# Kernel tuning notes

Measured on AMD Instinct MI355X. Metric: run time of the kernel, lower is better.

Reference implementation:

```python
import jax, jax.numpy as jnp
import numpy as np

N = 50000        # num nodes
E = 800000       # num edges (before self loops)
IN = 128         # in_channels
HID = 64         # hidden_channels
HEADS = 3        # num_heads
OUT = 32         # out_channels
SLOPE = 0.2      # PyG GATConv default negative_slope
HC = HEADS * HID


def setup_inputs() -> dict:
    key = jax.random.key(0)
    ks = jax.random.split(key, 12)

    def glorot(k, shape, fan_in):
        return jax.random.normal(k, shape, dtype=jnp.float32) / np.float32(np.sqrt(fan_in))

    x = jax.random.normal(ks[0], (N, IN), dtype=jnp.float32)
    edge_index = jax.random.randint(ks[1], (2, E), 0, N, dtype=jnp.int32)
    return {
        "x": x,
        "edge_index": edge_index,
        "W1": glorot(ks[2], (IN, HC), IN),
        "a_src1": glorot(ks[3], (HEADS, HID), HID),
        "a_dst1": glorot(ks[4], (HEADS, HID), HID),
        "b1": jnp.zeros((HC,), jnp.float32),
        "W2": glorot(ks[5], (HC, HC), HC),
        "a_src2": glorot(ks[6], (HEADS, HID), HID),
        "a_dst2": glorot(ks[7], (HEADS, HID), HID),
        "b2": jnp.zeros((HC,), jnp.float32),
        "Wf1": glorot(ks[8], (HC, 64), HC),
        "bf1": jnp.zeros((64,), jnp.float32),
        "Wf2": glorot(ks[9], (64, OUT), 64),
        "bf2": jnp.zeros((OUT,), jnp.float32),
        "num_nodes": N,
    }


def gat_conv(x, src, dst, W, a_src, a_dst, b, num_nodes):
    """PyG-style GATConv: linear -> edge score (LeakyReLU) -> segment softmax
    over incoming edges per destination -> weighted scatter-sum -> concat heads."""
    H, C = a_src.shape
    h = (x @ W).reshape(num_nodes, H, C)              # [N,H,C]
    alpha_s = jnp.einsum("nhc,hc->nh", h, a_src)      # [N,H]
    alpha_d = jnp.einsum("nhc,hc->nh", h, a_dst)      # [N,H]
    e = jax.nn.leaky_relu(alpha_s[src] + alpha_d[dst], SLOPE)  # [E',H]
    # numerically stable segment softmax over destination nodes
    m = jax.lax.stop_gradient(jax.ops.segment_max(e, dst, num_segments=num_nodes))
    ex = jnp.exp(e - m[dst])
    denom = jax.ops.segment_sum(ex, dst, num_segments=num_nodes)
    alpha = ex / (denom[dst] + 1e-16)                 # [E',H]
    msg = h[src] * alpha[:, :, None]                  # [E',H,C]
    out = jax.ops.segment_sum(msg, dst, num_segments=num_nodes)  # [N,H,C]
    return out.reshape(num_nodes, H * C) + b


def reference(x, edge_index, W1, a_src1, a_dst1, b1, W2, a_src2, a_dst2, b2,
              Wf1, bf1, Wf2, bf2, num_nodes):
    # add self loops (PyG GATConv default)
    loops = jnp.arange(num_nodes, dtype=edge_index.dtype)
    src = jnp.concatenate([edge_index[0], loops])
    dst = jnp.concatenate([edge_index[1], loops])

    h = gat_conv(x, src, dst, W1, a_src1, a_dst1, b1, num_nodes)
    h = jax.nn.elu(h)
    # dropout is identity in eval mode
    h = gat_conv(h, src, dst, W2, a_src2, a_dst2, b2, num_nodes)
    h = jax.nn.elu(h)
    h = h @ Wf1 + bf1
    return h @ Wf2 + bf2
```

## Files before the change

kernel.cpp:

```cpp
#include <hip/hip_runtime.h>

#define N_NODES 50000
#define E_EDGES 800000
#define EP (E_EDGES + N_NODES)
#define IN_CH 128
#define HID 64
#define HEADS 3
#define HC 192
#define OUT_CH 32
#define SLOPE 0.2f

#define N4 12500
#define SCAN_BLK 49

#define MB_XCONV 6250
#define MB_W1 (MB_XCONV + 96)
#define MB_W2 (MB_W1 + 144)
#define MB_FOLD (MB_W2 + 25)
#define MB_HIST (MB_FOLD + 3321)

typedef __attribute__((ext_vector_type(8))) short bf16x8;
typedef __attribute__((ext_vector_type(4))) float f32x4;

__device__ __forceinline__ unsigned short f2bf(float f) {
    unsigned int u = __float_as_uint(f);
    u = (u + 0x7fffu + ((u >> 16) & 1u)) >> 16;
    return (unsigned short)u;
}
__device__ __forceinline__ float loF(unsigned int u) { return __uint_as_float(u << 16); }
__device__ __forceinline__ float hiF(unsigned int u) { return __uint_as_float(u & 0xFFFF0000u); }


__global__ __launch_bounds__(256) void mega_pre_kernel(
    const float* __restrict__ x, unsigned short* __restrict__ xb,
    const float* __restrict__ W1, unsigned short* __restrict__ W1T,
    const float* __restrict__ W2, unsigned short* __restrict__ W2T,
    const float* __restrict__ Wf1, const float* __restrict__ bf1,
    const float* __restrict__ Wf2, const float* __restrict__ bf2,
    float* __restrict__ Wf, float* __restrict__ bf,
    const int* __restrict__ ei, int* __restrict__ cnt) {
    int b = blockIdx.x, t = threadIdx.x;
    if (b < MB_XCONV) {
        int i = b * 256 + t;
        float4 v = ((const float4*)x)[i];
        uint2 o;
        o.x = (unsigned int)f2bf(v.x) | ((unsigned int)f2bf(v.y) << 16);
        o.y = (unsigned int)f2bf(v.z) | ((unsigned int)f2bf(v.w) << 16);
        ((uint2*)xb)[i] = o;
    } else if (b < MB_W1) {
        int bb = b - MB_XCONV;
        int k = (bb & 3) * 32 + (t & 31);
        int n = (bb >> 2) * 8 + (t >> 5);
        W1T[n * IN_CH + k] = f2bf(W1[(size_t)k * HC + n]);
    } else if (b < MB_W2) {
        int bb = b - MB_W1;
        int k = (bb % 6) * 32 + (t & 31);
        int n = (bb / 6) * 8 + (t >> 5);
        W2T[n * HC + k] = f2bf(W2[(size_t)k * HC + n]);
    } else if (b < MB_FOLD) {
        int id = (b - MB_W2) * 256 + t;
        if (id < HC * OUT_CH) {
            int i = id / OUT_CH, j = id % OUT_CH;
            float s = 0.f;
            for (int k = 0; k < 64; ++k) s += Wf1[i * 64 + k] * Wf2[k * OUT_CH + j];
            Wf[id] = s;
        } else if (id < HC * OUT_CH + OUT_CH) {
            int j = id - HC * OUT_CH;
            float s = bf2[j];
            for (int k = 0; k < 64; ++k) s += bf1[k] * Wf2[k * OUT_CH + j];
            bf[j] = s;
        }
    } else {
        int i = (b - MB_FOLD) * 256 + t;
        if (i < EP) {
            int d = (i < E_EDGES) ? ei[E_EDGES + i] : (i - E_EDGES);
            atomicAdd(&cnt[d], 1);
        }
    }
}


__global__ __launch_bounds__(256) void scan_local_kernel(int* __restrict__ cnt,
                                                         int* __restrict__ offs,
                                                         int* __restrict__ bsum) {
    __shared__ int s[256];
    int t = threadIdx.x;
    int g = blockIdx.x * 256 + t;
    int4 v = make_int4(0, 0, 0, 0);
    if (g < N4) v = ((const int4*)cnt)[g];
    int sum = v.x + v.y + v.z + v.w;
    s[t] = sum; __syncthreads();
    #pragma unroll
    for (int o = 1; o < 256; o <<= 1) {
        int u = (t >= o) ? s[t - o] : 0;
        __syncthreads();
        s[t] += u;
        __syncthreads();
    }
    int ex = s[t] - sum;
    if (g < N4) {
        int4 w;
        w.x = ex;
        w.y = ex + v.x;
        w.z = ex + v.x + v.y;
        w.w = ex + v.x + v.y + v.z;
        ((int4*)offs)[g] = w;
        ((int4*)cnt)[g] = make_int4(0, 0, 0, 0);
    }
    if (t == 255) bsum[blockIdx.x] = s[255];
}

__global__ __launch_bounds__(256) void scan_add_kernel(int* __restrict__ offs,
                                                       const int* __restrict__ bsum) {
    int lane = threadIdx.x & 63;
    int orig = (lane < SCAN_BLK) ? bsum[lane] : 0;
    int v = orig;
    #pragma unroll
    for (int o = 1; o < 64; o <<= 1) {
        int u = __shfl_up(v, o);
        if (lane >= o) v += u;
    }
    int add = __shfl(v, blockIdx.x) - __shfl(orig, blockIdx.x);
    int total = __shfl(v, SCAN_BLK - 1);
    int g = blockIdx.x * 256 + threadIdx.x;
    if (g < N4) {
        int4 w = ((int4*)offs)[g];
        w.x += add; w.y += add; w.z += add; w.w += add;
        ((int4*)offs)[g] = w;
    }
    if (blockIdx.x == 0 && threadIdx.x == 0) offs[N_NODES] = total;
}

__global__ void scatter_kernel(const int* __restrict__ ei, const int* __restrict__ offs,
                               int* __restrict__ cnt, int* __restrict__ src_sort) {
    int i = blockIdx.x * 256 + threadIdx.x;
    if (i >= EP) return;
    int s_, d_;
    if (i < E_EDGES) { s_ = ei[i]; d_ = ei[E_EDGES + i]; }
    else             { s_ = d_ = i - E_EDGES; }
    int slot = atomicAdd(&cnt[d_], 1);
    src_sort[offs[d_] + slot] = s_;
}


#define GBM 128
#define GBK 64
#define LDA 72
#define CS_STR 200

template <int K>
__global__ __launch_bounds__(256) void gemm_mfma_kernel(
    const unsigned short* __restrict__ Ab, const unsigned short* __restrict__ Wt,
    const float* __restrict__ a_src, const float* __restrict__ a_dst,
    unsigned short* __restrict__ Hb, float* __restrict__ AS, float* __restrict__ AD) {
    __shared__ __align__(16) unsigned char smem[51200];
    unsigned short (*As)[LDA] = (unsigned short (*)[LDA])smem;
    unsigned short (*Bs)[LDA] = (unsigned short (*)[LDA])(smem + GBM * LDA * 2);
    int tid = threadIdx.x;
    int wid = tid >> 6, lane = tid & 63;
    int l15 = lane & 15, l4 = lane >> 4;
    int m0 = blockIdx.x * GBM;
    int sr = tid >> 3, sc = (tid & 7) * 8;

    f32x4 acc[2][12];
    #pragma unroll
    for (int m = 0; m < 2; ++m)
        #pragma unroll
        for (int n = 0; n < 12; ++n) acc[m][n] = (f32x4){0.f, 0.f, 0.f, 0.f};

    for (int kb = 0; kb < K; kb += GBK) {
        #pragma unroll
        for (int i = 0; i < 4; ++i) {
            int r = sr + 32 * i, grow = m0 + r;
            uint4 v = make_uint4(0, 0, 0, 0);
            if (grow < N_NODES) v = *(const uint4*)&Ab[(size_t)grow * K + kb + sc];
            *(uint4*)&As[r][sc] = v;
        }
        #pragma unroll
        for (int i = 0; i < 6; ++i) {
            int n = sr + 32 * i;
            uint4 v = *(const uint4*)&Wt[(size_t)n * K + kb + sc];
            *(uint4*)&Bs[n][sc] = v;
        }
        __syncthreads();
        #pragma unroll
        for (int ks = 0; ks < 2; ++ks) {
            int ko = ks * 32 + l4 * 8;
            bf16x8 a0 = *(const bf16x8*)&As[wid * 32 + l15][ko];
            bf16x8 a1 = *(const bf16x8*)&As[wid * 32 + 16 + l15][ko];
            #pragma unroll
            for (int n = 0; n < 12; ++n) {
                bf16x8 b = *(const bf16x8*)&Bs[n * 16 + l15][ko];
                acc[0][n] = __builtin_amdgcn_mfma_f32_16x16x32_bf16(a0, b, acc[0][n], 0, 0, 0);
                acc[1][n] = __builtin_amdgcn_mfma_f32_16x16x32_bf16(a1, b, acc[1][n], 0, 0, 0);
            }
        }
        __syncthreads();
    }

    float asv[12], adv[12];
    #pragma unroll
    for (int n = 0; n < 12; ++n) {
        asv[n] = a_src[n * 16 + l15];
        adv[n] = a_dst[n * 16 + l15];
    }
    #pragma unroll
    for (int m = 0; m < 2; ++m)
        #pragma unroll
        for (int r = 0; r < 4; ++r) {
            float ps[3], pd[3];
            #pragma unroll
            for (int h = 0; h < 3; ++h) {
                float s = 0.f, d = 0.f;
                #pragma unroll
                for (int j = 0; j < 4; ++j) {
                    float v = acc[m][4 * h + j][r];
                    s += v * asv[4 * h + j];
                    d += v * adv[4 * h + j];
                }
                #pragma unroll
                for (int o = 1; o < 16; o <<= 1) { s += __shfl_xor(s, o); d += __shfl_xor(d, o); }
                ps[h] = s; pd[h] = d;
            }
            if (l15 == 0) {
                int grow = m0 + wid * 32 + m * 16 + l4 * 4 + r;
                if (grow < N_NODES) {
                    #pragma unroll
                    for (int h = 0; h < 3; ++h) {
                        AS[grow * 3 + h] = ps[h];
                        AD[grow * 3 + h] = pd[h];
                    }
                }
            }
        }

    unsigned short* Cw = (unsigned short*)smem + wid * 32 * CS_STR;
    #pragma unroll
    for (int m = 0; m < 2; ++m)
        #pragma unroll
        for (int n = 0; n < 12; ++n)
            #pragma unroll
            for (int r = 0; r < 4; ++r)
                Cw[(m * 16 + l4 * 4 + r) * CS_STR + n * 16 + l15] = f2bf(acc[m][n][r]);
    __syncthreads();
    #pragma unroll
    for (int i = 0; i < 12; ++i) {
        int c = lane + 64 * i;
        int row = c / 24, off = c % 24;
        int grow = m0 + wid * 32 + row;
        if (grow < N_NODES) {
            uint4 v = *(const uint4*)&Cw[row * CS_STR + off * 8];
            *(uint4*)&Hb[(size_t)grow * HC + off * 8] = v;
        }
    }
}


__global__ __launch_bounds__(256) void aggregate_kernel(
    const int* __restrict__ src_sort, const int* __restrict__ offs,
    const float* __restrict__ AS, const float* __restrict__ AD,
    const unsigned short* __restrict__ Hb, const float* __restrict__ bias,
    unsigned short* __restrict__ Aout) {
    int w = blockIdx.x * 4 + (threadIdx.x >> 6);
    if (w >= N_NODES) return;
    int lane = threadIdx.x & 63;
    int g = lane >> 4, l = lane & 15, h3 = lane & 3;
    int beg = offs[w], end = offs[w + 1];

    float mx = -1e30f;
    for (int p0 = beg; p0 < end; p0 += 16) {
        int p = p0 + (lane >> 2);
        bool vld = (p < end) && (h3 < 3);
        int s_ = vld ? src_sort[p] : 0;
        float a = vld ? AS[s_ * 3 + h3] : -1e30f;
        mx = fmaxf(mx, a);
    }
    mx = fmaxf(mx, __shfl_xor(mx, 4));
    mx = fmaxf(mx, __shfl_xor(mx, 8));
    mx = fmaxf(mx, __shfl_xor(mx, 16));
    mx = fmaxf(mx, __shfl_xor(mx, 32));
    float ad = (l < 3) ? AD[w * 3 + l] : 0.f;
    float sm = mx + ad;
    float m = fmaxf(sm, SLOPE * sm);

    int c0 = l * 12;
    int h0 = c0 >> 6, h1 = (c0 + 4) >> 6, h2 = (c0 + 8) >> 6;
    float A0 = 0.f, A1 = 0.f, A2 = 0.f, A3 = 0.f;
    float B0 = 0.f, B1 = 0.f, B2 = 0.f, B3 = 0.f;
    float C0 = 0.f, C1 = 0.f, C2 = 0.f, C3 = 0.f;
    float den = 0.f;

    for (int p0 = beg; p0 < end; p0 += 4) {
        int p = p0 + g;
        bool pv = p < end;
        int pc = pv ? p : end - 1;
        int s_ = src_sort[pc];
        float e = 0.f;
        if (l < 3) {
            float v = AS[s_ * 3 + l] + ad;
            v = fmaxf(v, SLOPE * v);
            e = pv ? __expf(v - m) : 0.f;
        }
        den += e;
        float w0 = __shfl(e, g * 16 + h0);
        float w1 = __shfl(e, g * 16 + h1);
        float w2 = __shfl(e, g * 16 + h2);
        const unsigned short* hr = Hb + (unsigned)s_ * HC + c0;
        uint2 v0 = *(const uint2*)hr;
        uint2 v1 = *(const uint2*)(hr + 4);
        uint2 v2 = *(const uint2*)(hr + 8);
        A0 += w0 * loF(v0.x); A1 += w0 * hiF(v0.x); A2 += w0 * loF(v0.y); A3 += w0 * hiF(v0.y);
        B0 += w1 * loF(v1.x); B1 += w1 * hiF(v1.x); B2 += w1 * loF(v1.y); B3 += w1 * hiF(v1.y);
        C0 += w2 * loF(v2.x); C1 += w2 * hiF(v2.x); C2 += w2 * loF(v2.y); C3 += w2 * hiF(v2.y);
    }

    #pragma unroll
    for (int o = 16; o < 64; o <<= 1) {
        A0 += __shfl_xor(A0, o); A1 += __shfl_xor(A1, o); A2 += __shfl_xor(A2, o); A3 += __shfl_xor(A3, o);
        B0 += __shfl_xor(B0, o); B1 += __shfl_xor(B1, o); B2 += __shfl_xor(B2, o); B3 += __shfl_xor(B3, o);
        C0 += __shfl_xor(C0, o); C1 += __shfl_xor(C1, o); C2 += __shfl_xor(C2, o); C3 += __shfl_xor(C3, o);
        den += __shfl_xor(den, o);
    }
    float i0 = 1.f / (__shfl(den, h0) + 1e-16f);
    float i1 = 1.f / (__shfl(den, h1) + 1e-16f);
    float i2 = 1.f / (__shfl(den, h2) + 1e-16f);

    if (lane < 16) {
        float4 bi0 = *(const float4*)&bias[c0];
        float4 bi1 = *(const float4*)&bias[c0 + 4];
        float4 bi2 = *(const float4*)&bias[c0 + 8];
        A0 = A0 * i0 + bi0.x; A1 = A1 * i0 + bi0.y; A2 = A2 * i0 + bi0.z; A3 = A3 * i0 + bi0.w;
        B0 = B0 * i1 + bi1.x; B1 = B1 * i1 + bi1.y; B2 = B2 * i1 + bi1.z; B3 = B3 * i1 + bi1.w;
        C0 = C0 * i2 + bi2.x; C1 = C1 * i2 + bi2.y; C2 = C2 * i2 + bi2.z; C3 = C3 * i2 + bi2.w;
        A0 = (A0 > 0.f) ? A0 : (__expf(A0) - 1.f);
        A1 = (A1 > 0.f) ? A1 : (__expf(A1) - 1.f);
        A2 = (A2 > 0.f) ? A2 : (__expf(A2) - 1.f);
        A3 = (A3 > 0.f) ? A3 : (__expf(A3) - 1.f);
        B0 = (B0 > 0.f) ? B0 : (__expf(B0) - 1.f);
        B1 = (B1 > 0.f) ? B1 : (__expf(B1) - 1.f);
        B2 = (B2 > 0.f) ? B2 : (__expf(B2) - 1.f);
        B3 = (B3 > 0.f) ? B3 : (__expf(B3) - 1.f);
        C0 = (C0 > 0.f) ? C0 : (__expf(C0) - 1.f);
        C1 = (C1 > 0.f) ? C1 : (__expf(C1) - 1.f);
        C2 = (C2 > 0.f) ? C2 : (__expf(C2) - 1.f);
        C3 = (C3 > 0.f) ? C3 : (__expf(C3) - 1.f);
        unsigned short* op = Aout + (size_t)w * HC + c0;
        uint2 o0, o1, o2;
        o0.x = (unsigned int)f2bf(A0) | ((unsigned int)f2bf(A1) << 16);
        o0.y = (unsigned int)f2bf(A2) | ((unsigned int)f2bf(A3) << 16);
        o1.x = (unsigned int)f2bf(B0) | ((unsigned int)f2bf(B1) << 16);
        o1.y = (unsigned int)f2bf(B2) | ((unsigned int)f2bf(B3) << 16);
        o2.x = (unsigned int)f2bf(C0) | ((unsigned int)f2bf(C1) << 16);
        o2.y = (unsigned int)f2bf(C2) | ((unsigned int)f2bf(C3) << 16);
        *(uint2*)op = o0;
        *(uint2*)(op + 4) = o1;
        *(uint2*)(op + 8) = o2;
    }
}


__global__ __launch_bounds__(256) void mlp_kernel(const unsigned short* __restrict__ act,
                                                  const float* __restrict__ Wf,
                                                  const float* __restrict__ bf,
                                                  float* __restrict__ out) {
    __shared__ float sW[HC * OUT_CH];
    __shared__ float sA[32 * 193];
    __shared__ float sb[OUT_CH];
    int tid = threadIdx.x;
    for (int i = tid; i < HC * OUT_CH; i += 256) sW[i] = Wf[i];
    if (tid < OUT_CH) sb[tid] = bf[tid];
    int n0 = blockIdx.x * 32;
    for (int i = tid; i < 32 * HC / 4; i += 256) {
        int r = i / 48, c4 = i % 48;
        int n = n0 + r;
        uint2 v = make_uint2(0, 0);
        if (n < N_NODES) v = *(const uint2*)&act[(size_t)n * HC + c4 * 4];
        float* dst = &sA[r * 193 + c4 * 4];
        dst[0] = loF(v.x); dst[1] = hiF(v.x); dst[2] = loF(v.y); dst[3] = hiF(v.y);
    }
    __syncthreads();
    int r = tid >> 3, jg = tid & 7;
    float a0 = sb[jg * 4 + 0], a1 = sb[jg * 4 + 1], a2 = sb[jg * 4 + 2], a3 = sb[jg * 4 + 3];
    #pragma unroll 4
    for (int k = 0; k < HC; ++k) {
        float xv = sA[r * 193 + k];
        float4 wv = *(const float4*)&sW[k * OUT_CH + jg * 4];
        a0 += xv * wv.x; a1 += xv * wv.y; a2 += xv * wv.z; a3 += xv * wv.w;
    }
    int n = n0 + r;
    if (n < N_NODES) {
        float4 v = make_float4(a0, a1, a2, a3);
        *(float4*)&out[(size_t)n * OUT_CH + jg * 4] = v;
    }
}


extern "C" void kernel_launch(void* const* d_in, const int* in_sizes, int n_in,
                              void* d_out, int out_size, void* d_ws, size_t ws_size,
                              hipStream_t stream) {
    (void)in_sizes; (void)n_in; (void)out_size; (void)ws_size;
    const float* x   = (const float*)d_in[0];
    const int*   ei  = (const int*)d_in[1];
    const float* W1  = (const float*)d_in[2];
    const float* as1 = (const float*)d_in[3];
    const float* ad1 = (const float*)d_in[4];
    const float* b1  = (const float*)d_in[5];
    const float* W2  = (const float*)d_in[6];
    const float* as2 = (const float*)d_in[7];
    const float* ad2 = (const float*)d_in[8];
    const float* b2  = (const float*)d_in[9];
    const float* Wf1 = (const float*)d_in[10];
    const float* bf1 = (const float*)d_in[11];
    const float* Wf2 = (const float*)d_in[12];
    const float* bf2 = (const float*)d_in[13];
    float* out = (float*)d_out;

    char* ws = (char*)d_ws;
    size_t off = 0;
    auto alloc = [&](size_t b) { size_t o = off; off += (b + 255) & ~(size_t)255; return o; };
    unsigned short* XB  = (unsigned short*)(ws + alloc((size_t)N_NODES * IN_CH * 2));
    unsigned short* W1T = (unsigned short*)(ws + alloc((size_t)HC * IN_CH * 2));
    unsigned short* W2T = (unsigned short*)(ws + alloc((size_t)HC * HC * 2));
    unsigned short* HB  = (unsigned short*)(ws + alloc((size_t)N_NODES * HC * 2));
    unsigned short* ACT = (unsigned short*)(ws + alloc((size_t)N_NODES * HC * 2));
    int*   SRC  = (int*)  (ws + alloc((size_t)(EP + 64) * 4));
    float* AS   = (float*)(ws + alloc((size_t)N_NODES * 3 * 4));
    float* AD   = (float*)(ws + alloc((size_t)N_NODES * 3 * 4));
    int*   OFFS = (int*)  (ws + alloc((size_t)(N_NODES + 4) * 4));
    int*   CNT  = (int*)  (ws + alloc((size_t)N_NODES * 4));
    int*   BSUM = (int*)  (ws + alloc((size_t)256 * 4));
    float* WF   = (float*)(ws + alloc((size_t)HC * OUT_CH * 4));
    float* BF   = (float*)(ws + alloc((size_t)OUT_CH * 4));

    int eb = (EP + 255) / 256;
    int gmb = (N_NODES + GBM - 1) / GBM;

    hipMemsetAsync(CNT, 0, (size_t)N_NODES * 4, stream);
    mega_pre_kernel<<<MB_HIST, 256, 0, stream>>>(x, XB, W1, W1T, W2, W2T,
                                                 Wf1, bf1, Wf2, bf2, WF, BF, ei, CNT);
    scan_local_kernel<<<SCAN_BLK, 256, 0, stream>>>(CNT, OFFS, BSUM);
    scan_add_kernel<<<SCAN_BLK, 256, 0, stream>>>(OFFS, BSUM);
    scatter_kernel<<<eb, 256, 0, stream>>>(ei, OFFS, CNT, SRC);

    gemm_mfma_kernel<IN_CH><<<gmb, 256, 0, stream>>>(XB, W1T, as1, ad1, HB, AS, AD);
    aggregate_kernel<<<(N_NODES + 3) / 4, 256, 0, stream>>>(SRC, OFFS, AS, AD, HB, b1, ACT);
    gemm_mfma_kernel<HC><<<gmb, 256, 0, stream>>>(ACT, W2T, as2, ad2, HB, AS, AD);
    aggregate_kernel<<<(N_NODES + 3) / 4, 256, 0, stream>>>(SRC, OFFS, AS, AD, HB, b2, ACT);
    mlp_kernel<<<(N_NODES + 31) / 32, 256, 0, stream>>>(ACT, WF, BF, out);
}
```

Before: 307.4 us.

## Split GAT aggregation across heads with one wave per node-head pair

The aggregation kernel now launches one wavefront per (node, head) instead of one per node. Each lane group accumulates a 4-channel slice of a single head, and the next source index is prefetched one iteration ahead. This removes the shuffles that broadcast weights across heads and wastes fewer lanes on exp work, while giving three times as many waves for latency hiding. The cost is that src_sort and the offsets are re-read three times, and each gather touches only an 8-byte slice of the bf16 row, so cache line use per wave is poorer.

```diff
diff --git a/kernel.cpp b/kernel.cpp
--- a/kernel.cpp
+++ b/kernel.cpp
@@ -12,6 +12,7 @@
 
 #define N4 12500
 #define SCAN_BLK 49
+#define NGRP 12500
 
 #define MB_XCONV 6250
 #define MB_W1 (MB_XCONV + 96)
@@ -261,100 +262,64 @@
     const float* __restrict__ AS, const float* __restrict__ AD,
     const unsigned short* __restrict__ Hb, const float* __restrict__ bias,
     unsigned short* __restrict__ Aout) {
-    int w = blockIdx.x * 4 + (threadIdx.x >> 6);
-    if (w >= N_NODES) return;
+    int h = blockIdx.x / NGRP;
+    int g4 = blockIdx.x - h * NGRP;
+    int w = g4 * 4 + (threadIdx.x >> 6);
     int lane = threadIdx.x & 63;
-    int g = lane >> 4, l = lane & 15, h3 = lane & 3;
+    int slot = lane >> 4, l = lane & 15;
     int beg = offs[w], end = offs[w + 1];
+    float ad = AD[w * 3 + h];
 
     float mx = -1e30f;
-    for (int p0 = beg; p0 < end; p0 += 16) {
-        int p = p0 + (lane >> 2);
-        bool vld = (p < end) && (h3 < 3);
-        int s_ = vld ? src_sort[p] : 0;
-        float a = vld ? AS[s_ * 3 + h3] : -1e30f;
-        mx = fmaxf(mx, a);
-    }
-    mx = fmaxf(mx, __shfl_xor(mx, 4));
-    mx = fmaxf(mx, __shfl_xor(mx, 8));
-    mx = fmaxf(mx, __shfl_xor(mx, 16));
-    mx = fmaxf(mx, __shfl_xor(mx, 32));
-    float ad = (l < 3) ? AD[w * 3 + l] : 0.f;
+    for (int p = beg + lane; p < end; p += 64) {
+        int s_ = src_sort[p];
+        mx = fmaxf(mx, AS[s_ * 3 + h]);
+    }
+    #pragma unroll
+    for (int o = 1; o < 64; o <<= 1) mx = fmaxf(mx, __shfl_xor(mx, o));
     float sm = mx + ad;
     float m = fmaxf(sm, SLOPE * sm);
 
-    int c0 = l * 12;
-    int h0 = c0 >> 6, h1 = (c0 + 4) >> 6, h2 = (c0 + 8) >> 6;
-    float A0 = 0.f, A1 = 0.f, A2 = 0.f, A3 = 0.f;
-    float B0 = 0.f, B1 = 0.f, B2 = 0.f, B3 = 0.f;
-    float C0 = 0.f, C1 = 0.f, C2 = 0.f, C3 = 0.f;
-    float den = 0.f;
-
+    int coff = h * 64 + l * 4;
+    float a0 = 0.f, a1 = 0.f, a2 = 0.f, a3 = 0.f, den = 0.f;
+    int p = beg + slot;
+    int s_ = src_sort[(p < end) ? p : (end - 1)];
     for (int p0 = beg; p0 < end; p0 += 4) {
-        int p = p0 + g;
-        bool pv = p < end;
-        int pc = pv ? p : end - 1;
-        int s_ = src_sort[pc];
-        float e = 0.f;
-        if (l < 3) {
-            float v = AS[s_ * 3 + l] + ad;
-            v = fmaxf(v, SLOPE * v);
-            e = pv ? __expf(v - m) : 0.f;
-        }
+        int pn = p0 + 4 + slot;
+        int sn = src_sort[(pn < end) ? pn : (end - 1)];
+        bool pv = (p0 + slot) < end;
+        float v = AS[s_ * 3 + h] + ad;
+        v = fmaxf(v, SLOPE * v);
+        float e = pv ? __expf(v - m) : 0.f;
         den += e;
-        float w0 = __shfl(e, g * 16 + h0);
-        float w1 = __shfl(e, g * 16 + h1);
-        float w2 = __shfl(e, g * 16 + h2);
-        const unsigned short* hr = Hb + (unsigned)s_ * HC + c0;
-        uint2 v0 = *(const uint2*)hr;
-        uint2 v1 = *(const uint2*)(hr + 4);
-        uint2 v2 = *(const uint2*)(hr + 8);
-        A0 += w0 * loF(v0.x); A1 += w0 * hiF(v0.x); A2 += w0 * loF(v0.y); A3 += w0 * hiF(v0.y);
-        B0 += w1 * loF(v1.x); B1 += w1 * hiF(v1.x); B2 += w1 * loF(v1.y); B3 += w1 * hiF(v1.y);
-        C0 += w2 * loF(v2.x); C1 += w2 * hiF(v2.x); C2 += w2 * loF(v2.y); C3 += w2 * hiF(v2.y);
+        uint2 hv = *(const uint2*)&Hb[(unsigned)s_ * HC + coff];
+        a0 += e * loF(hv.x); a1 += e * hiF(hv.x);
+        a2 += e * loF(hv.y); a3 += e * hiF(hv.y);
+        s_ = sn;
     }
 
     #pragma unroll
     for (int o = 16; o < 64; o <<= 1) {
-        A0 += __shfl_xor(A0, o); A1 += __shfl_xor(A1, o); A2 += __shfl_xor(A2, o); A3 += __shfl_xor(A3, o);
-        B0 += __shfl_xor(B0, o); B1 += __shfl_xor(B1, o); B2 += __shfl_xor(B2, o); B3 += __shfl_xor(B3, o);
-        C0 += __shfl_xor(C0, o); C1 += __shfl_xor(C1, o); C2 += __shfl_xor(C2, o); C3 += __shfl_xor(C3, o);
+        a0 += __shfl_xor(a0, o); a1 += __shfl_xor(a1, o);
+        a2 += __shfl_xor(a2, o); a3 += __shfl_xor(a3, o);
         den += __shfl_xor(den, o);
     }
-    float i0 = 1.f / (__shfl(den, h0) + 1e-16f);
-    float i1 = 1.f / (__shfl(den, h1) + 1e-16f);
-    float i2 = 1.f / (__shfl(den, h2) + 1e-16f);
 
     if (lane < 16) {
-        float4 bi0 = *(const float4*)&bias[c0];
-        float4 bi1 = *(const float4*)&bias[c0 + 4];
-        float4 bi2 = *(const float4*)&bias[c0 + 8];
-        A0 = A0 * i0 + bi0.x; A1 = A1 * i0 + bi0.y; A2 = A2 * i0 + bi0.z; A3 = A3 * i0 + bi0.w;
-        B0 = B0 * i1 + bi1.x; B1 = B1 * i1 + bi1.y; B2 = B2 * i1 + bi1.z; B3 = B3 * i1 + bi1.w;
-        C0 = C0 * i2 + bi2.x; C1 = C1 * i2 + bi2.y; C2 = C2 * i2 + bi2.z; C3 = C3 * i2 + bi2.w;
-        A0 = (A0 > 0.f) ? A0 : (__expf(A0) - 1.f);
-        A1 = (A1 > 0.f) ? A1 : (__expf(A1) - 1.f);
-        A2 = (A2 > 0.f) ? A2 : (__expf(A2) - 1.f);
-        A3 = (A3 > 0.f) ? A3 : (__expf(A3) - 1.f);
-        B0 = (B0 > 0.f) ? B0 : (__expf(B0) - 1.f);
-        B1 = (B1 > 0.f) ? B1 : (__expf(B1) - 1.f);
-        B2 = (B2 > 0.f) ? B2 : (__expf(B2) - 1.f);
-        B3 = (B3 > 0.f) ? B3 : (__expf(B3) - 1.f);
-        C0 = (C0 > 0.f) ? C0 : (__expf(C0) - 1.f);
-        C1 = (C1 > 0.f) ? C1 : (__expf(C1) - 1.f);
-        C2 = (C2 > 0.f) ? C2 : (__expf(C2) - 1.f);
-        C3 = (C3 > 0.f) ? C3 : (__expf(C3) - 1.f);
-        unsigned short* op = Aout + (size_t)w * HC + c0;
-        uint2 o0, o1, o2;
-        o0.x = (unsigned int)f2bf(A0) | ((unsigned int)f2bf(A1) << 16);
-        o0.y = (unsigned int)f2bf(A2) | ((unsigned int)f2bf(A3) << 16);
-        o1.x = (unsigned int)f2bf(B0) | ((unsigned int)f2bf(B1) << 16);
-        o1.y = (unsigned int)f2bf(B2) | ((unsigned int)f2bf(B3) << 16);
-        o2.x = (unsigned int)f2bf(C0) | ((unsigned int)f2bf(C1) << 16);
-        o2.y = (unsigned int)f2bf(C2) | ((unsigned int)f2bf(C3) << 16);
-        *(uint2*)op = o0;
-        *(uint2*)(op + 4) = o1;
-        *(uint2*)(op + 8) = o2;
+        float inv = 1.f / (den + 1e-16f);
+        float4 bi = *(const float4*)&bias[coff];
+        a0 = a0 * inv + bi.x;
+        a1 = a1 * inv + bi.y;
+        a2 = a2 * inv + bi.z;
+        a3 = a3 * inv + bi.w;
+        a0 = (a0 > 0.f) ? a0 : (__expf(a0) - 1.f);
+        a1 = (a1 > 0.f) ? a1 : (__expf(a1) - 1.f);
+        a2 = (a2 > 0.f) ? a2 : (__expf(a2) - 1.f);
+        a3 = (a3 > 0.f) ? a3 : (__expf(a3) - 1.f);
+        uint2 o;
+        o.x = (unsigned int)f2bf(a0) | ((unsigned int)f2bf(a1) << 16);
+        o.y = (unsigned int)f2bf(a2) | ((unsigned int)f2bf(a3) << 16);
+        *(uint2*)&Aout[(size_t)w * HC + coff] = o;
     }
 }
 
@@ -443,8 +408,8 @@
     scatter_kernel<<<eb, 256, 0, stream>>>(ei, OFFS, CNT, SRC);
 
     gemm_mfma_kernel<IN_CH><<<gmb, 256, 0, stream>>>(XB, W1T, as1, ad1, HB, AS, AD);
-    aggregate_kernel<<<(N_NODES + 3) / 4, 256, 0, stream>>>(SRC, OFFS, AS, AD, HB, b1, ACT);
+    aggregate_kernel<<<HEADS * NGRP, 256, 0, stream>>>(SRC, OFFS, AS, AD, HB, b1, ACT);
     gemm_mfma_kernel<HC><<<gmb, 256, 0, stream>>>(ACT, W2T, as2, ad2, HB, AS, AD);
-    aggregate_kernel<<<(N_NODES + 3) / 4, 256, 0, stream>>>(SRC, OFFS, AS, AD, HB, b2, ACT);
+    aggregate_kernel<<<HEADS * NGRP, 256, 0, stream>>>(SRC, OFFS, AS, AD, HB, b2, ACT);
     mlp_kernel<<<(N_NODES + 31) / 32, 256, 0, stream>>>(ACT, WF, BF, out);
 }
```

New measurement: 395.7 us. +28.7%, slower.

## Use global per-head max for softmax shift and prefetch next edge in aggregation

Applied to the files above, without the earlier changes.

The GEMM epilogue now reduces the source attention scores to a per-head global maximum and publishes it with an order-preserving-key atomicMax. The aggregation kernel uses that bound as the softmax shift instead of running a separate per-destination max pass over incoming edges, which removes one full gather sweep over src_sort and AS. The aggregation loop is also software-pipelined: the next edge's source index and exp weight are fetched while the current edge's features are accumulated. Shifting by a global rather than per-node max is mathematically equivalent but risks exp underflow when a node's scores sit far below the global maximum.

```diff
diff --git a/kernel.cpp b/kernel.cpp
--- a/kernel.cpp
+++ b/kernel.cpp
@@ -29,6 +29,15 @@
 }
 __device__ __forceinline__ float loF(unsigned int u) { return __uint_as_float(u << 16); }
 __device__ __forceinline__ float hiF(unsigned int u) { return __uint_as_float(u & 0xFFFF0000u); }
+
+__device__ __forceinline__ unsigned int fkey(float f) {
+    unsigned int u = __float_as_uint(f);
+    return (u & 0x80000000u) ? ~u : (u | 0x80000000u);
+}
+__device__ __forceinline__ float unfkey(unsigned int k) {
+    unsigned int u = (k & 0x80000000u) ? (k ^ 0x80000000u) : ~k;
+    return __uint_as_float(u);
+}
 
 
 __global__ __launch_bounds__(256) void mega_pre_kernel(
@@ -152,8 +161,10 @@
 __global__ __launch_bounds__(256) void gemm_mfma_kernel(
     const unsigned short* __restrict__ Ab, const unsigned short* __restrict__ Wt,
     const float* __restrict__ a_src, const float* __restrict__ a_dst,
-    unsigned short* __restrict__ Hb, float* __restrict__ AS, float* __restrict__ AD) {
+    unsigned short* __restrict__ Hb, float* __restrict__ AS, float* __restrict__ AD,
+    unsigned int* __restrict__ mk) {
     __shared__ __align__(16) unsigned char smem[51200];
+    __shared__ float pmx[4][3];
     unsigned short (*As)[LDA] = (unsigned short (*)[LDA])smem;
     unsigned short (*Bs)[LDA] = (unsigned short (*)[LDA])(smem + GBM * LDA * 2);
     int tid = threadIdx.x;
@@ -204,6 +215,7 @@
         asv[n] = a_src[n * 16 + l15];
         adv[n] = a_dst[n * 16 + l15];
     }
+    float pm[3] = {-1e30f, -1e30f, -1e30f};
     #pragma unroll
     for (int m = 0; m < 2; ++m)
         #pragma unroll
@@ -221,6 +233,7 @@
                 #pragma unroll
                 for (int o = 1; o < 16; o <<= 1) { s += __shfl_xor(s, o); d += __shfl_xor(d, o); }
                 ps[h] = s; pd[h] = d;
+                pm[h] = fmaxf(pm[h], s);
             }
             if (l15 == 0) {
                 int grow = m0 + wid * 32 + m * 16 + l4 * 4 + r;
@@ -233,6 +246,12 @@
                 }
             }
         }
+    #pragma unroll
+    for (int h = 0; h < 3; ++h) {
+        pm[h] = fmaxf(pm[h], __shfl_xor(pm[h], 16));
+        pm[h] = fmaxf(pm[h], __shfl_xor(pm[h], 32));
+    }
+    if (lane == 0) { pmx[wid][0] = pm[0]; pmx[wid][1] = pm[1]; pmx[wid][2] = pm[2]; }
 
     unsigned short* Cw = (unsigned short*)smem + wid * 32 * CS_STR;
     #pragma unroll
@@ -253,35 +272,30 @@
             *(uint4*)&Hb[(size_t)grow * HC + off * 8] = v;
         }
     }
+    if (tid < 3) {
+        float bm = fmaxf(fmaxf(pmx[0][tid], pmx[1][tid]), fmaxf(pmx[2][tid], pmx[3][tid]));
+        atomicMax(&mk[tid], fkey(bm));
+    }
 }
 
 
 __global__ __launch_bounds__(256) void aggregate_kernel(
     const int* __restrict__ src_sort, const int* __restrict__ offs,
     const float* __restrict__ AS, const float* __restrict__ AD,
+    const unsigned int* __restrict__ mkey,
     const unsigned short* __restrict__ Hb, const float* __restrict__ bias,
     unsigned short* __restrict__ Aout) {
     int w = blockIdx.x * 4 + (threadIdx.x >> 6);
-    if (w >= N_NODES) return;
     int lane = threadIdx.x & 63;
-    int g = lane >> 4, l = lane & 15, h3 = lane & 3;
+    int g = lane >> 4, l = lane & 15;
     int beg = offs[w], end = offs[w + 1];
 
-    float mx = -1e30f;
-    for (int p0 = beg; p0 < end; p0 += 16) {
-        int p = p0 + (lane >> 2);
-        bool vld = (p < end) && (h3 < 3);
-        int s_ = vld ? src_sort[p] : 0;
-        float a = vld ? AS[s_ * 3 + h3] : -1e30f;
-        mx = fmaxf(mx, a);
-    }
-    mx = fmaxf(mx, __shfl_xor(mx, 4));
-    mx = fmaxf(mx, __shfl_xor(mx, 8));
-    mx = fmaxf(mx, __shfl_xor(mx, 16));
-    mx = fmaxf(mx, __shfl_xor(mx, 32));
-    float ad = (l < 3) ? AD[w * 3 + l] : 0.f;
-    float sm = mx + ad;
-    float m = fmaxf(sm, SLOPE * sm);
+    float ad = 0.f, m = 0.f;
+    if (l < 3) {
+        ad = AD[w * 3 + l];
+        float sm = unfkey(mkey[l]) + ad;
+        m = fmaxf(sm, SLOPE * sm);
+    }
 
     int c0 = l * 12;
     int h0 = c0 >> 6, h1 = (c0 + 4) >> 6, h2 = (c0 + 8) >> 6;
@@ -290,28 +304,37 @@
     float C0 = 0.f, C1 = 0.f, C2 = 0.f, C3 = 0.f;
     float den = 0.f;
 
+    int p = beg + g;
+    bool pv = p < end;
+    int s_ = src_sort[pv ? p : (end - 1)];
+    float e_;
+    {
+        float v = (l < 3) ? (AS[s_ * 3 + l] + ad) : 0.f;
+        v = fmaxf(v, SLOPE * v);
+        e_ = (pv && l < 3) ? __expf(v - m) : 0.f;
+    }
     for (int p0 = beg; p0 < end; p0 += 4) {
-        int p = p0 + g;
-        bool pv = p < end;
-        int pc = pv ? p : end - 1;
-        int s_ = src_sort[pc];
-        float e = 0.f;
-        if (l < 3) {
-            float v = AS[s_ * 3 + l] + ad;
-            v = fmaxf(v, SLOPE * v);
-            e = pv ? __expf(v - m) : 0.f;
-        }
-        den += e;
-        float w0 = __shfl(e, g * 16 + h0);
-        float w1 = __shfl(e, g * 16 + h1);
-        float w2 = __shfl(e, g * 16 + h2);
+        int pn = p0 + 4 + g;
+        bool pnv = pn < end;
+        int sn = src_sort[pnv ? pn : (end - 1)];
         const unsigned short* hr = Hb + (unsigned)s_ * HC + c0;
         uint2 v0 = *(const uint2*)hr;
         uint2 v1 = *(const uint2*)(hr + 4);
         uint2 v2 = *(const uint2*)(hr + 8);
+        float en;
+        {
+            float v = (l < 3) ? (AS[sn * 3 + l] + ad) : 0.f;
+            v = fmaxf(v, SLOPE * v);
+            en = (pnv && l < 3) ? __expf(v - m) : 0.f;
+        }
+        den += e_;
+        float w0 = __shfl(e_, g * 16 + h0);
+        float w1 = __shfl(e_, g * 16 + h1);
+        float w2 = __shfl(e_, g * 16 + h2);
         A0 += w0 * loF(v0.x); A1 += w0 * hiF(v0.x); A2 += w0 * loF(v0.y); A3 += w0 * hiF(v0.y);
         B0 += w1 * loF(v1.x); B1 += w1 * hiF(v1.x); B2 += w1 * loF(v1.y); B3 += w1 * hiF(v1.y);
         C0 += w2 * loF(v2.x); C1 += w2 * hiF(v2.x); C2 += w2 * loF(v2.y); C3 += w2 * hiF(v2.y);
+        s_ = sn; e_ = en;
     }
 
     #pragma unroll
@@ -427,7 +450,8 @@
     float* AS   = (float*)(ws + alloc((size_t)N_NODES * 3 * 4));
     float* AD   = (float*)(ws + alloc((size_t)N_NODES * 3 * 4));
     int*   OFFS = (int*)  (ws + alloc((size_t)(N_NODES + 4) * 4));
-    int*   CNT  = (int*)  (ws + alloc((size_t)N_NODES * 4));
+    int*   CNT  = (int*)  (ws + alloc((size_t)(N_NODES + 16) * 4));
+    unsigned int* MKEY = (unsigned int*)(CNT + N_NODES);
     int*   BSUM = (int*)  (ws + alloc((size_t)256 * 4));
     float* WF   = (float*)(ws + alloc((size_t)HC * OUT_CH * 4));
     float* BF   = (float*)(ws + alloc((size_t)OUT_CH * 4));
@@ -435,16 +459,16 @@
     int eb = (EP + 255) / 256;
     int gmb = (N_NODES + GBM - 1) / GBM;
 
-    hipMemsetAsync(CNT, 0, (size_t)N_NODES * 4, stream);
+    hipMemsetAsync(CNT, 0, (size_t)(N_NODES + 16) * 4, stream);
     mega_pre_kernel<<<MB_HIST, 256, 0, stream>>>(x, XB, W1, W1T, W2, W2T,
                                                  Wf1, bf1, Wf2, bf2, WF, BF, ei, CNT);
     scan_local_kernel<<<SCAN_BLK, 256, 0, stream>>>(CNT, OFFS, BSUM);
     scan_add_kernel<<<SCAN_BLK, 256, 0, stream>>>(OFFS, BSUM);
     scatter_kernel<<<eb, 256, 0, stream>>>(ei, OFFS, CNT, SRC);
 
-    gemm_mfma_kernel<IN_CH><<<gmb, 256, 0, stream>>>(XB, W1T, as1, ad1, HB, AS, AD);
-    aggregate_kernel<<<(N_NODES + 3) / 4, 256, 0, stream>>>(SRC, OFFS, AS, AD, HB, b1, ACT);
-    gemm_mfma_kernel<HC><<<gmb, 256, 0, stream>>>(ACT, W2T, as2, ad2, HB, AS, AD);
-    aggregate_kernel<<<(N_NODES + 3) / 4, 256, 0, stream>>>(SRC, OFFS, AS, AD, HB, b2, ACT);
+    gemm_mfma_kernel<IN_CH><<<gmb, 256, 0, stream>>>(XB, W1T, as1, ad1, HB, AS, AD, MKEY);
+    aggregate_kernel<<<(N_NODES + 3) / 4, 256, 0, stream>>>(SRC, OFFS, AS, AD, MKEY, HB, b1, ACT);
+    gemm_mfma_kernel<HC><<<gmb, 256, 0, stream>>>(ACT, W2T, as2, ad2, HB, AS, AD, MKEY + 3);
+    aggregate_kernel<<<(N_NODES + 3) / 4, 256, 0, stream>>>(SRC, OFFS, AS, AD, MKEY + 3, HB, b2, ACT);
     mlp_kernel<<<(N_NODES + 31) / 32, 256, 0, stream>>>(ACT, WF, BF, out);
 }
```

Result: faster. 292.6 us (-4.8%).
